# Kernel tuning notes

Measured on AMD Instinct MI355X. Metric: run time of the kernel, lower is better.

## Reference

```python
import jax, jax.numpy as jnp
import numpy as np

B, T, F_IN = 64, 396, 128
D_MODEL, N_HEAD, D_QKV, D_FF = 768, 8, 96, 3072
N_LAYERS, N_OUT, REL_D = 6, 256, 100


def setup_inputs():
    key = jax.random.key(0)
    cnt = [0]
    def rn(shape, std=1.0):
        cnt[0] += 1
        return jax.random.normal(jax.random.fold_in(key, cnt[0]), shape, jnp.float32) * std
    inp = {"x_raw": rn((B, T, F_IN))}
    def add_rb(p, cin, cout):
        inp[p + "_c1_w"] = rn((cout, cin, 3), (2.0 / (cin * 3)) ** 0.5)
        inp[p + "_c1_b"] = rn((cout,), 0.01)
        inp[p + "_bn1_s"] = 1.0 + rn((cout,), 0.1)
        inp[p + "_bn1_b"] = rn((cout,), 0.1)
        inp[p + "_c2_w"] = rn((cout, cout, 3), (2.0 / (cout * 3)) ** 0.5)
        inp[p + "_c2_b"] = rn((cout,), 0.01)
        inp[p + "_bn2_s"] = 1.0 + rn((cout,), 0.1)
        inp[p + "_bn2_b"] = rn((cout,), 0.1)
        inp[p + "_cr_w"] = rn((cout, cin, 1), (2.0 / cin) ** 0.5)
        inp[p + "_cr_b"] = rn((cout,), 0.01)
        inp[p + "_bnr_s"] = 1.0 + rn((cout,), 0.1)
        inp[p + "_bnr_b"] = rn((cout,), 0.1)
    add_rb("rb1", F_IN, D_MODEL)
    add_rb("rb2", D_MODEL, D_MODEL)
    inp["w_in_w"] = rn((D_MODEL, D_MODEL), D_MODEL ** -0.5)
    inp["w_in_b"] = rn((D_MODEL,), 0.01)
    inp["cls_token"] = jnp.zeros((1, 1, D_MODEL), jnp.float32)
    xav = (2.0 / (D_MODEL + D_QKV)) ** 0.5
    inp["wq"] = rn((N_LAYERS, N_HEAD, D_MODEL, D_QKV), xav)
    inp["wk"] = rn((N_LAYERS, N_HEAD, D_MODEL, D_QKV), xav)
    inp["wv"] = rn((N_LAYERS, N_HEAD, D_MODEL, D_QKV), xav)
    inp["wo"] = rn((N_LAYERS, N_HEAD, D_QKV, D_MODEL), xav)
    inp["rel_emb"] = rn((N_LAYERS, N_HEAD, 2 * REL_D + 1, D_QKV), D_QKV ** -0.5)
    inp["ln1_g"] = jnp.ones((N_LAYERS, D_MODEL), jnp.float32)
    inp["ln1_b"] = jnp.zeros((N_LAYERS, D_MODEL), jnp.float32)
    inp["ln2_g"] = jnp.ones((N_LAYERS, D_MODEL), jnp.float32)
    inp["ln2_b"] = jnp.zeros((N_LAYERS, D_MODEL), jnp.float32)
    inp["ff1_w"] = rn((N_LAYERS, D_FF, D_MODEL), (2.0 / D_MODEL) ** 0.5)
    inp["ff1_b"] = rn((N_LAYERS, D_FF), 0.01)
    inp["ff2_w"] = rn((N_LAYERS, D_MODEL, D_FF), (1.0 / D_FF) ** 0.5)
    inp["ff2_b"] = rn((N_LAYERS, D_MODEL), 0.01)
    inp["w_out_w"] = rn((N_OUT, D_MODEL), D_MODEL ** -0.5)
    inp["w_out_b"] = rn((N_OUT,), 0.01)
    return inp


def _conv1d(x, w, b, stride=1):
    # x: [B, Cin, T], w: [Cout, Cin, K]
    pad = (w.shape[-1] - 1) // 2
    y = jax.lax.conv_general_dilated(x, w, (stride,), [(pad, pad)],
                                     dimension_numbers=("NCH", "OIH", "NCH"))
    return y + b[None, :, None]


def _bn(x, s, b):
    # eval-mode BatchNorm1d folded into per-channel affine
    return x * s[None, :, None] + b[None, :, None]


def _resblock(x, c1w, c1b, s1, b1, c2w, c2b, s2, b2, crw, crb, sr, br, stride):
    h = jax.nn.relu(_bn(_conv1d(x, c1w, c1b, stride), s1, b1))
    h = _bn(_conv1d(h, c2w, c2b), s2, b2)
    r = _bn(_conv1d(x, crw, crb, stride), sr, br)
    return jax.nn.relu(h + r)


def _layer_norm(x, g, b, eps=1e-5):
    m = jnp.mean(x, -1, keepdims=True)
    v = jnp.mean((x - m) ** 2, -1, keepdims=True)
    return (x - m) * jax.lax.rsqrt(v + eps) * g + b


def _attention(x, wq, wk, wv, wo, rel):
    # x: [B, L, D]; relative-positional attention (fairseq LearnedRelativePositionalEmbedding, unmasked)
    L = x.shape[1]
    q = jnp.einsum("btf,hfa->bhta", x, wq) * (D_QKV ** -0.5)
    k = jnp.einsum("btf,hfa->bhta", x, wk)
    v = jnp.einsum("btf,hfa->bhta", x, wv)
    logits = jnp.einsum("bhqa,bhka->bhqk", q, k)
    # narrow embeddings to the 2L-1 relative positions used (L <= REL_D)
    start = REL_D - L
    rel_used = rel[:, start:start + 2 * L - 1, :]  # [h, 2L-1, a]
    pos_all = jnp.einsum("bhqa,hma->bhqm", q, rel_used)  # [B,h,L,2L-1]
    idx = jnp.arange(L)[None, :] - jnp.arange(L)[:, None] + (L - 1)  # [L,L], rel->abs skew
    logits = logits + jnp.take_along_axis(pos_all, idx[None, None], axis=3)
    probs = jax.nn.softmax(logits, axis=-1)
    o = jnp.einsum("bhqk,bhka->bhqa", probs, v)
    return jnp.einsum("bhta,haf->btf", o, wo)


def reference(x_raw, rb1_c1_w, rb1_c1_b, rb1_bn1_s, rb1_bn1_b, rb1_c2_w, rb1_c2_b, rb1_bn2_s, rb1_bn2_b, rb1_cr_w, rb1_cr_b, rb1_bnr_s, rb1_bnr_b, rb2_c1_w, rb2_c1_b, rb2_bn1_s, rb2_bn1_b, rb2_c2_w, rb2_c2_b, rb2_bn2_s, rb2_bn2_b, rb2_cr_w, rb2_cr_b, rb2_bnr_s, rb2_bnr_b, w_in_w, w_in_b, cls_token, wq, wk, wv, wo, rel_emb, ln1_g, ln1_b, ln2_g, ln2_b, ff1_w, ff1_b, ff2_w, ff2_b, w_out_w, w_out_b):
    x = jnp.transpose(x_raw, (0, 2, 1))  # [B, F_IN, T]
    x = _resblock(x, rb1_c1_w, rb1_c1_b, rb1_bn1_s, rb1_bn1_b, rb1_c2_w, rb1_c2_b, rb1_bn2_s, rb1_bn2_b, rb1_cr_w, rb1_cr_b, rb1_bnr_s, rb1_bnr_b, 2)
    x = _resblock(x, rb2_c1_w, rb2_c1_b, rb2_bn1_s, rb2_bn1_b, rb2_c2_w, rb2_c2_b, rb2_bn2_s, rb2_bn2_b, rb2_cr_w, rb2_cr_b, rb2_bnr_s, rb2_bnr_b, 2)
    x = jnp.transpose(x, (0, 2, 1))  # [B, T', D]
    x = x @ w_in_w.T + w_in_b
    cls = jnp.broadcast_to(cls_token, (x.shape[0], 1, D_MODEL))
    x = jnp.concatenate([cls, x], axis=1)  # [B, L, D], L = T'+1
    for l in range(N_LAYERS):
        a = _attention(x, wq[l], wk[l], wv[l], wo[l], rel_emb[l])
        x = _layer_norm(x + a, ln1_g[l], ln1_b[l])
        h = jax.nn.relu(x @ ff1_w[l].T + ff1_b[l]) @ ff2_w[l].T + ff2_b[l]
        x = _layer_norm(x + h, ln2_g[l], ln2_b[l])
    return x[:, 0, :] @ w_out_w.T + w_out_b
```

## Files before the change

kernel.cpp:

```cpp
#include <hip/hip_runtime.h>

typedef _Float16 h8 __attribute__((ext_vector_type(8)));
typedef float f4 __attribute__((ext_vector_type(4)));

namespace {

constexpr int DM   = 768;
constexpr int NHEAD= 8;
constexpr int DQ   = 96;
constexpr int DFF  = 3072;
constexpr int NL   = 6;
constexpr int B_   = 64;
constexpr int T0   = 396, T1 = 198, T2 = 99;
constexpr int FIN  = 128;
constexpr int L_   = 100;
constexpr int MSEQ = B_ * L_;
constexpr int M1   = B_ * T1;
constexpr int M2   = B_ * T2;
constexpr int NREL = 201;
constexpr int POSN = 256;
constexpr int RELK = 128;

enum { EPI_F32 = 0, EPI_RELU_H, EPI_H, EPI_CONV_BN_H, EPI_CONV_RELU_H, EPI_CONV_ADD_RELU_H };

__device__ __forceinline__ void g2l16(const _Float16* g, _Float16* l)
{
    __builtin_amdgcn_global_load_lds(
        (const __attribute__((address_space(1))) unsigned int*)g,
        (__attribute__((address_space(3))) unsigned int*)l,
        16, 0, 0);
}

template<int EPI, bool OPAD, int MI>
__device__ __forceinline__ void epilogue(
    f4 (&acc)[MI][4], int lane, int m0, int wm, int n0, int wn,
    int M, int N, int T_out, int bz,
    float* Cf, _Float16* Ch, const float* bias, const float* bns,
    const float* bnb, const _Float16* res, size_t c_z)
{
    const int frc = lane & 15;
    const int fq4 = (lane >> 4) * 4;
    float*    Cfo = Cf ? Cf + (size_t)bz * c_z : nullptr;
    _Float16* Cho = Ch ? Ch + (size_t)bz * c_z : nullptr;
    #pragma unroll
    for (int mi = 0; mi < MI; ++mi)
        #pragma unroll
        for (int ni = 0; ni < 4; ++ni)
            #pragma unroll
            for (int r = 0; r < 4; ++r) {
                int row = m0 + wm + mi * 16 + fq4 + r;
                int col = n0 + wn + ni * 16 + frc;
                if (row >= M) continue;
                float v = acc[mi][ni][r];
                size_t roff;
                if (OPAD) {
                    int ab = row / T_out, at = row - ab * T_out;
                    roff = ((size_t)ab * (T_out + 2) + at + 1) * N + col;
                } else {
                    roff = (size_t)row * N + col;
                }
                if (EPI == EPI_F32) {
                    if (bias) v += bias[col];
                    Cfo[roff] = v;
                } else if (EPI == EPI_RELU_H) {
                    if (bias) v += bias[col];
                    Cho[roff] = (_Float16)fmaxf(v, 0.0f);
                } else if (EPI == EPI_H) {
                    Cho[roff] = (_Float16)v;
                } else if (EPI == EPI_CONV_BN_H) {
                    v = bns[col] * (v + bias[col]) + bnb[col];
                    Cho[roff] = (_Float16)v;
                } else if (EPI == EPI_CONV_RELU_H) {
                    v = bns[col] * (v + bias[col]) + bnb[col];
                    Cho[roff] = (_Float16)fmaxf(v, 0.0f);
                } else {
                    v = bns[col] * (v + bias[col]) + bnb[col]
                      + (float)res[(size_t)row * N + col];
                    Cho[roff] = (_Float16)fmaxf(v, 0.0f);
                }
            }
}

template<int EPI, bool OPAD, int MI>
__global__ __launch_bounds__(256)
void gemm5_k(const _Float16* __restrict__ A, const _Float16* __restrict__ B,
             float* __restrict__ Cf, _Float16* __restrict__ Ch,
             const float* __restrict__ bias, const float* __restrict__ bns,
             const float* __restrict__ bnb, const _Float16* __restrict__ res,
             int M, int N, int K, int lda,
             int T_out, int Tp_in, int stride_t, int KS, int in_off,
             int gx, int gxy)
{
    constexpr int TM = MI * 32;
    __shared__ _Float16 As[TM * 64];
    __shared__ _Float16 Bs[128 * 64];

    const unsigned nwg = gridDim.x, orig = blockIdx.x;
    const unsigned q = nwg >> 3, rr_ = nwg & 7;
    const unsigned xcd = orig & 7, idx = orig >> 3;
    const unsigned wgid = (xcd < rr_) ? xcd * (q + 1) + idx
                                      : rr_ * (q + 1) + (xcd - rr_) * q + idx;
    const int by  = (int)(wgid / (unsigned)gx);
    const int bx  = (int)(wgid - (unsigned)by * (unsigned)gx);
    (void)gxy;

    const int tid  = threadIdx.x;
    const int lane = tid & 63;
    const int wid  = tid >> 6;
    const int m0   = by * TM;
    const int n0   = bx * 128;
    const int wm   = (wid >> 1) * (MI * 16);
    const int wn   = (wid & 1) * 64;

    f4 acc[MI][4];
    #pragma unroll
    for (int i = 0; i < MI; ++i)
        #pragma unroll
        for (int j = 0; j < 4; ++j)
            #pragma unroll
            for (int p = 0; p < 4; ++p) acc[i][j][p] = 0.0f;

    const int colh = (((lane & 7) ^ ((lane >> 3) & 7)) << 3);
    size_t aoff[MI];
    #pragma unroll
    for (int i = 0; i < MI; ++i) {
        int m = min(m0 + wid * (MI * 8) + i * 8 + (lane >> 3), M - 1);
        int ab = m / T_out, at = m - ab * T_out;
        aoff[i] = ((size_t)ab * Tp_in + at * stride_t + in_off) * lda + colh;
    }
    size_t boff[4];
    #pragma unroll
    for (int i = 0; i < 4; ++i)
        boff[i] = (size_t)(n0 + wid * 32 + i * 8 + (lane >> 3)) * K + colh;
    const size_t bdk = (size_t)N * K;

    const int fr  = lane & 15;
    const int grp = lane >> 4;

    for (int dk = 0; dk < KS; ++dk) {
        const size_t adk = (size_t)dk * lda;
        const size_t bdo = (size_t)dk * bdk;

        for (int k0 = 0; k0 < K; k0 += 64) {
            #pragma unroll
            for (int i = 0; i < MI; ++i)
                g2l16(A + aoff[i] + adk + k0, &As[(wid * (MI * 8) + i * 8) * 64]);
            #pragma unroll
            for (int i = 0; i < 4; ++i)
                g2l16(B + boff[i] + bdo + k0, &Bs[(wid * 32 + i * 8) * 64]);
            __syncthreads();

            #pragma unroll
            for (int kh = 0; kh < 2; ++kh) {
                const int co = (((kh * 4 + grp) ^ (fr & 7)) << 3);
                h8 af[MI], bf[4];
                #pragma unroll
                for (int mi = 0; mi < MI; ++mi)
                    af[mi] = *(const h8*)&As[(wm + mi * 16 + fr) * 64 + co];
                #pragma unroll
                for (int ni = 0; ni < 4; ++ni)
                    bf[ni] = *(const h8*)&Bs[(wn + ni * 16 + fr) * 64 + co];
                #pragma unroll
                for (int mi = 0; mi < MI; ++mi)
                    #pragma unroll
                    for (int ni = 0; ni < 4; ++ni)
                        acc[mi][ni] = __builtin_amdgcn_mfma_f32_16x16x32_f16(
                            af[mi], bf[ni], acc[mi][ni], 0, 0, 0);
            }
            __syncthreads();
        }
    }

    epilogue<EPI, OPAD, MI>(acc, lane, m0, wm, n0, wn, M, N, T_out, 0,
                            Cf, Ch, bias, bns, bnb, res, 0);
}

template<int EPI, int MI>
__global__ __launch_bounds__(256)
void gemm6_k(const _Float16* __restrict__ A, const _Float16* __restrict__ B,
             float* __restrict__ Cf, _Float16* __restrict__ Ch,
             const float* __restrict__ bias,
             int M, int N, int K, int lda,
             int gx, int gxy,
             size_t a_z, size_t b_z, size_t c_z)
{
    constexpr int TM = MI * 32;
    __shared__ _Float16 As[2][TM * 64];
    __shared__ _Float16 Bs[2][128 * 64];

    const unsigned nwg = gridDim.x, orig = blockIdx.x;
    const unsigned q = nwg >> 3, rr_ = nwg & 7;
    const unsigned xcd = orig & 7, idx = orig >> 3;
    const unsigned wgid = (xcd < rr_) ? xcd * (q + 1) + idx
                                      : rr_ * (q + 1) + (xcd - rr_) * q + idx;
    const int bz  = (int)(wgid / (unsigned)gxy);
    const int rem = (int)(wgid - (unsigned)bz * (unsigned)gxy);
    const int by  = rem / gx;
    const int bx  = rem - by * gx;

    A += (size_t)bz * a_z;
    B += (size_t)bz * b_z;

    const int tid  = threadIdx.x;
    const int lane = tid & 63;
    const int wid  = tid >> 6;
    const int m0   = by * TM;
    const int n0   = bx * 128;
    const int wm   = (wid >> 1) * (MI * 16);
    const int wn   = (wid & 1) * 64;

    f4 acc[MI][4];
    #pragma unroll
    for (int i = 0; i < MI; ++i)
        #pragma unroll
        for (int j = 0; j < 4; ++j)
            #pragma unroll
            for (int p = 0; p < 4; ++p) acc[i][j][p] = 0.0f;

    const int colh = (((lane & 7) ^ ((lane >> 3) & 7)) << 3);
    size_t aoff[MI];
    #pragma unroll
    for (int i = 0; i < MI; ++i) {
        int m = min(m0 + wid * (MI * 8) + i * 8 + (lane >> 3), M - 1);
        aoff[i] = (size_t)m * lda + colh;
    }
    size_t boff[4];
    #pragma unroll
    for (int i = 0; i < 4; ++i)
        boff[i] = (size_t)(n0 + wid * 32 + i * 8 + (lane >> 3)) * K + colh;

    const int fr  = lane & 15;
    const int grp = lane >> 4;
    const int NS  = K >> 6;

    auto stage = [&](int step, int buf) {
        const int k0 = step << 6;
        #pragma unroll
        for (int i = 0; i < MI; ++i)
            g2l16(A + aoff[i] + k0, &As[buf][(wid * (MI * 8) + i * 8) * 64]);
        #pragma unroll
        for (int i = 0; i < 4; ++i)
            g2l16(B + boff[i] + k0, &Bs[buf][(wid * 32 + i * 8) * 64]);
    };

    stage(0, 0);
    __syncthreads();

    for (int step = 0; step < NS; ++step) {
        const int cur = step & 1;
        const _Float16* As_ = As[cur];
        const _Float16* Bs_ = Bs[cur];

        const int co0 = ((grp ^ (fr & 7)) << 3);
        h8 af0[MI], bf0[4];
        #pragma unroll
        for (int mi = 0; mi < MI; ++mi)
            af0[mi] = *(const h8*)&As_[(wm + mi * 16 + fr) * 64 + co0];
        #pragma unroll
        for (int ni = 0; ni < 4; ++ni)
            bf0[ni] = *(const h8*)&Bs_[(wn + ni * 16 + fr) * 64 + co0];

        if (step + 1 < NS) stage(step + 1, cur ^ 1);

        #pragma unroll
        for (int mi = 0; mi < MI; ++mi)
            #pragma unroll
            for (int ni = 0; ni < 4; ++ni)
                acc[mi][ni] = __builtin_amdgcn_mfma_f32_16x16x32_f16(
                    af0[mi], bf0[ni], acc[mi][ni], 0, 0, 0);

        const int co1 = (((4 + grp) ^ (fr & 7)) << 3);
        h8 af1[MI], bf1[4];
        #pragma unroll
        for (int mi = 0; mi < MI; ++mi)
            af1[mi] = *(const h8*)&As_[(wm + mi * 16 + fr) * 64 + co1];
        #pragma unroll
        for (int ni = 0; ni < 4; ++ni)
            bf1[ni] = *(const h8*)&Bs_[(wn + ni * 16 + fr) * 64 + co1];
        #pragma unroll
        for (int mi = 0; mi < MI; ++mi)
            #pragma unroll
            for (int ni = 0; ni < 4; ++ni)
                acc[mi][ni] = __builtin_amdgcn_mfma_f32_16x16x32_f16(
                    af1[mi], bf1[ni], acc[mi][ni], 0, 0, 0);

        __syncthreads();
    }

    epilogue<EPI, false, MI>(acc, lane, m0, wm, n0, wn, M, N, 0, bz,
                             Cf, Ch, bias, nullptr, nullptr, nullptr, c_z);
}


__global__ void f2h_k(const float* __restrict__ in, _Float16* __restrict__ out,
                      long n, float scale)
{
    long i = (long)blockIdx.x * blockDim.x + threadIdx.x;
    if (i < n) out[i] = (_Float16)(in[i] * scale);
}

__global__ void f2h8_k(const float* __restrict__ in, _Float16* __restrict__ out,
                       long n8)
{
    long i = (long)blockIdx.x * blockDim.x + threadIdx.x;
    if (i >= n8) return;
    f4 a = ((const f4*)in)[2 * i];
    f4 b = ((const f4*)in)[2 * i + 1];
    h8 o;
    #pragma unroll
    for (int j = 0; j < 4; ++j) { o[j] = (_Float16)a[j]; o[4 + j] = (_Float16)b[j]; }
    ((h8*)out)[i] = o;
}

__global__ void f2h_pad_k(const float* __restrict__ in, _Float16* __restrict__ out)
{
    long i = (long)blockIdx.x * blockDim.x + threadIdx.x;
    if (i >= (long)B_ * 398 * FIN) return;
    int  c = (int)(i % FIN);
    long r = i / FIN;
    int  t = (int)(r % 398);
    int  b = (int)(r / 398);
    float v = (t == 0 || t == 397) ? 0.0f
            : in[((long)b * T0 + (t - 1)) * FIN + c];
    out[i] = (_Float16)v;
}

__global__ void zero_pad_k(_Float16* __restrict__ buf, int Tp, int C)
{
    long i = (long)blockIdx.x * blockDim.x + threadIdx.x;
    if (i >= (long)B_ * 2 * C) return;
    int  c = (int)(i % C);
    long r = i / C;
    int  hi = (int)(r % 2);
    int  b  = (int)(r / 2);
    buf[((size_t)b * Tp + (hi ? Tp - 1 : 0)) * C + c] = (_Float16)0.0f;
}

__global__ void pack_qkv_k(const float* __restrict__ wq, const float* __restrict__ wk,
                           const float* __restrict__ wv, _Float16* __restrict__ out)
{
    long i = (long)blockIdx.x * blockDim.x + threadIdx.x;
    if (i >= (long)NL * 2304 * DM) return;
    int  f = (int)(i % DM);
    long r = i / DM;
    int  n = (int)(r % 2304);
    int  l = (int)(r / 2304);
    int  s = n / DM, hn = n % DM, h = hn / DQ, a = hn % DQ;
    const float* src = (s == 0) ? wq : ((s == 1) ? wk : wv);
    out[i] = (_Float16)src[(((long)l * NHEAD + h) * DM + f) * DQ + a];
}

__global__ void pack_wo_k(const float* __restrict__ wo, _Float16* __restrict__ out)
{
    long i = (long)blockIdx.x * blockDim.x + threadIdx.x;
    if (i >= (long)NL * DM * DM) return;
    int  ha = (int)(i % DM);
    long r  = i / DM;
    int  f  = (int)(r % DM);
    int  l  = (int)(r / DM);
    int  h = ha / DQ, a = ha % DQ;
    out[i] = (_Float16)wo[(((long)l * NHEAD + h) * DQ + a) * DM + f];
}

__global__ void pack_conv_k(const float* __restrict__ w, _Float16* __restrict__ out,
                            int Cout, int Cin, int KS)
{
    long i = (long)blockIdx.x * blockDim.x + threadIdx.x;
    if (i >= (long)Cout * Cin * KS) return;
    int  ci = (int)(i % Cin);
    long r  = i / Cin;
    int  co = (int)(r % Cout);
    int  dk = (int)(r / Cout);
    out[i] = (_Float16)w[((long)co * Cin + ci) * KS + dk];
}

__global__ void pack_rel_k(const float* __restrict__ rel, _Float16* __restrict__ out)
{
    long i = (long)blockIdx.x * blockDim.x + threadIdx.x;
    if (i >= (long)NL * NHEAD * POSN * RELK) return;
    int  k = (int)(i & (RELK - 1));
    long r = i >> 7;
    int  n = (int)(r & (POSN - 1));
    long r2 = r >> 8;
    int  h = (int)(r2 & (NHEAD - 1));
    int  l = (int)(r2 >> 3);
    float v = 0.0f;
    if (n < NREL && k < DQ)
        v = rel[(((long)l * NHEAD + h) * NREL + n) * DQ + k] * 0.10206207261596575f;
    out[i] = (_Float16)v;
}

__global__ void concat_k(const float* __restrict__ xlin, const float* __restrict__ cls,
                         float* __restrict__ xf, _Float16* __restrict__ xh)
{
    long i = (long)blockIdx.x * blockDim.x + threadIdx.x;
    if (i >= (long)MSEQ * DM) return;
    int  c = (int)(i % DM);
    long m = i / DM;
    int  b = (int)(m / L_), t = (int)(m % L_);
    float v = (t == 0) ? cls[c] : xlin[((long)b * (L_ - 1) + (t - 1)) * DM + c];
    xf[i] = v;
    xh[i] = (_Float16)v;
}

__global__ __launch_bounds__(256)
void ln_k(const float* x, const float* __restrict__ d,
          const float* __restrict__ g, const float* __restrict__ bb,
          float* xo, _Float16* __restrict__ xh)
{
    long row = blockIdx.x;
    const float* xr = x + row * DM;
    const float* dr = d + row * DM;
    float v[3];
    float s = 0.0f;
    #pragma unroll
    for (int k = 0; k < 3; ++k) {
        int c = threadIdx.x + 256 * k;
        v[k] = xr[c] + dr[c];
        s += v[k];
    }
    __shared__ float red[8];
    #pragma unroll
    for (int o = 32; o; o >>= 1) s += __shfl_xor(s, o, 64);
    int w = threadIdx.x >> 6, lane = threadIdx.x & 63;
    if (lane == 0) red[w] = s;
    __syncthreads();
    s = red[0] + red[1] + red[2] + red[3];
    float mean = s * (1.0f / DM);
    float vs = 0.0f;
    #pragma unroll
    for (int k = 0; k < 3; ++k) { float t = v[k] - mean; vs += t * t; }
    #pragma unroll
    for (int o = 32; o; o >>= 1) vs += __shfl_xor(vs, o, 64);
    if (lane == 0) red[4 + w] = vs;
    __syncthreads();
    vs = red[4] + red[5] + red[6] + red[7];
    float rstd = rsqrtf(vs * (1.0f / DM) + 1e-5f);
    #pragma unroll
    for (int k = 0; k < 3; ++k) {
        int c = threadIdx.x + 256 * k;
        float y = (v[k] - mean) * rstd * g[c] + bb[c];
        xo[row * DM + c] = y;
        xh[row * DM + c] = (_Float16)y;
    }
}

constexpr int LP = 128;
constexpr int KP = 104;
constexpr int PP = 136;

__global__ __launch_bounds__(256)
void attn_k(const _Float16* __restrict__ qkv, const _Float16* __restrict__ pos,
            _Float16* __restrict__ o)
{
    __shared__ __align__(16) char smem[60928];
    _Float16* Ks = (_Float16*)smem;
    _Float16* Ps = (_Float16*)smem;
    _Float16* Vt = (_Float16*)(smem + 34816);

    const int h = blockIdx.x, b = blockIdx.y;
    const int tid = threadIdx.x, lane = tid & 63, w = tid >> 6;
    const _Float16* base = qkv + (size_t)b * L_ * 2304 + h * DQ;
    const float qscale = 0.10206207261596575f;

    {
        int row = tid >> 1;
        int c0  = (tid & 1) * 48;
        const bool real = row < L_;
        const _Float16* krow = base + 768 + (size_t)row * 2304;
        #pragma unroll
        for (int q = 0; q < 6; ++q) {
            int c = c0 + q * 8;
            h8 kv;
            #pragma unroll
            for (int e = 0; e < 8; ++e) kv[e] = (_Float16)0.0f;
            if (real) kv = *(const h8*)(krow + c);
            *(h8*)&Ks[row * KP + c] = kv;
        }
        for (int idx = tid; idx < DQ * LP; idx += 256) {
            int a = idx % DQ, j = idx / DQ;
            _Float16 v = (_Float16)0.0f;
            if (j < L_) v = base[1536 + (size_t)j * 2304 + a];
            Vt[a * PP + j] = v;
        }
    }
    __syncthreads();

    const int fr = lane & 15;
    const int fk = (lane >> 4) * 8;
    const int rbase = w * 32 + ((lane >> 4) << 2);

    f4 acc[2][8];
    #pragma unroll
    for (int mi = 0; mi < 2; ++mi)
        #pragma unroll
        for (int ni = 0; ni < 8; ++ni)
            #pragma unroll
            for (int q = 0; q < 4; ++q) acc[mi][ni][q] = 0.0f;

    #pragma unroll
    for (int k0 = 0; k0 < DQ; k0 += 32) {
        h8 a0 = *(const h8*)(base + (size_t)(w * 32 + fr) * 2304 + k0 + fk);
        h8 a1 = *(const h8*)(base + (size_t)(w * 32 + 16 + fr) * 2304 + k0 + fk);
        #pragma unroll
        for (int ni = 0; ni < 8; ++ni) {
            h8 bv = *(const h8*)&Ks[(ni * 16 + fr) * KP + k0 + fk];
            acc[0][ni] = __builtin_amdgcn_mfma_f32_16x16x32_f16(a0, bv, acc[0][ni], 0, 0, 0);
            acc[1][ni] = __builtin_amdgcn_mfma_f32_16x16x32_f16(a1, bv, acc[1][ni], 0, 0, 0);
        }
    }

    const _Float16* posb = pos + ((size_t)h * MSEQ + (size_t)b * L_) * POSN;
    #pragma unroll
    for (int mi = 0; mi < 2; ++mi)
        #pragma unroll
        for (int r = 0; r < 4; ++r) {
            int i = rbase + mi * 16 + r;
            float s[8];
            #pragma unroll
            for (int ni = 0; ni < 8; ++ni) {
                int j = ni * 16 + fr;
                float v = -3.0e38f;
                if (i < L_ && j < L_)
                    v = acc[mi][ni][r] * qscale
                      + (float)posb[(size_t)i * POSN + (j - i + (L_ - 1))];
                s[ni] = v;
            }
            float m = s[0];
            #pragma unroll
            for (int ni = 1; ni < 8; ++ni) m = fmaxf(m, s[ni]);
            #pragma unroll
            for (int msk = 1; msk < 16; msk <<= 1) m = fmaxf(m, __shfl_xor(m, msk, 64));
            float sum = 0.0f;
            #pragma unroll
            for (int ni = 0; ni < 8; ++ni) { s[ni] = __expf(s[ni] - m); sum += s[ni]; }
            #pragma unroll
            for (int msk = 1; msk < 16; msk <<= 1) sum += __shfl_xor(sum, msk, 64);
            float inv = 1.0f / sum;
            #pragma unroll
            for (int ni = 0; ni < 8; ++ni) acc[mi][ni][r] = s[ni] * inv;
        }

    __syncthreads();

    #pragma unroll
    for (int mi = 0; mi < 2; ++mi)
        #pragma unroll
        for (int r = 0; r < 4; ++r) {
            int i = rbase + mi * 16 + r;
            #pragma unroll
            for (int ni = 0; ni < 8; ++ni)
                Ps[i * PP + ni * 16 + fr] = (_Float16)acc[mi][ni][r];
        }
    __syncthreads();

    f4 acc2[2][6];
    #pragma unroll
    for (int mi = 0; mi < 2; ++mi)
        #pragma unroll
        for (int ni = 0; ni < 6; ++ni)
            #pragma unroll
            for (int q = 0; q < 4; ++q) acc2[mi][ni][q] = 0.0f;

    #pragma unroll
    for (int k0 = 0; k0 < LP; k0 += 32) {
        h8 a0 = *(const h8*)&Ps[(w * 32 + fr) * PP + k0 + fk];
        h8 a1 = *(const h8*)&Ps[(w * 32 + 16 + fr) * PP + k0 + fk];
        #pragma unroll
        for (int ni = 0; ni < 6; ++ni) {
            h8 bv = *(const h8*)&Vt[(ni * 16 + fr) * PP + k0 + fk];
            acc2[0][ni] = __builtin_amdgcn_mfma_f32_16x16x32_f16(a0, bv, acc2[0][ni], 0, 0, 0);
            acc2[1][ni] = __builtin_amdgcn_mfma_f32_16x16x32_f16(a1, bv, acc2[1][ni], 0, 0, 0);
        }
    }

    _Float16* ob = o + (size_t)b * L_ * DM + h * DQ;
    #pragma unroll
    for (int mi = 0; mi < 2; ++mi)
        #pragma unroll
        for (int r = 0; r < 4; ++r) {
            int i = rbase + mi * 16 + r;
            if (i < L_) {
                #pragma unroll
                for (int ni = 0; ni < 6; ++ni)
                    ob[(size_t)i * DM + ni * 16 + fr] = (_Float16)acc2[mi][ni][r];
            }
        }
}

__global__ __launch_bounds__(256)
void out_k(const float* __restrict__ xseq, const float* __restrict__ w,
           const float* __restrict__ bias, float* __restrict__ out)
{
    __shared__ float xs[DM];
    int b = blockIdx.x;
    for (int c = threadIdx.x; c < DM; c += 256) xs[c] = xseq[(size_t)b * L_ * DM + c];
    __syncthreads();
    int n = threadIdx.x;
    const f4* wr = (const f4*)(w + (size_t)n * DM);
    float acc = 0.0f;
    #pragma unroll 4
    for (int k4 = 0; k4 < DM / 4; ++k4) {
        f4 wv = wr[k4];
        f4 xv = *(const f4*)&xs[k4 * 4];
        acc += wv[0]*xv[0] + wv[1]*xv[1] + wv[2]*xv[2] + wv[3]*xv[3];
    }
    out[(size_t)b * 256 + n] = acc + bias[n];
}

}

extern "C" void kernel_launch(void* const* d_in, const int* in_sizes, int n_in,
                              void* d_out, int out_size, void* d_ws, size_t ws_size,
                              hipStream_t stream)
{
    (void)in_sizes; (void)n_in; (void)out_size; (void)ws_size;

    const float* x_raw   = (const float*)d_in[0];
    const float* rb1_c1w = (const float*)d_in[1];
    const float* rb1_c1b = (const float*)d_in[2];
    const float* rb1_s1  = (const float*)d_in[3];
    const float* rb1_b1  = (const float*)d_in[4];
    const float* rb1_c2w = (const float*)d_in[5];
    const float* rb1_c2b = (const float*)d_in[6];
    const float* rb1_s2  = (const float*)d_in[7];
    const float* rb1_b2  = (const float*)d_in[8];
    const float* rb1_crw = (const float*)d_in[9];
    const float* rb1_crb = (const float*)d_in[10];
    const float* rb1_sr  = (const float*)d_in[11];
    const float* rb1_br  = (const float*)d_in[12];
    const float* rb2_c1w = (const float*)d_in[13];
    const float* rb2_c1b = (const float*)d_in[14];
    const float* rb2_s1  = (const float*)d_in[15];
    const float* rb2_b1  = (const float*)d_in[16];
    const float* rb2_c2w = (const float*)d_in[17];
    const float* rb2_c2b = (const float*)d_in[18];
    const float* rb2_s2  = (const float*)d_in[19];
    const float* rb2_b2  = (const float*)d_in[20];
    const float* rb2_crw = (const float*)d_in[21];
    const float* rb2_crb = (const float*)d_in[22];
    const float* rb2_sr  = (const float*)d_in[23];
    const float* rb2_br  = (const float*)d_in[24];
    const float* w_in_w  = (const float*)d_in[25];
    const float* w_in_b  = (const float*)d_in[26];
    const float* cls     = (const float*)d_in[27];
    const float* wq      = (const float*)d_in[28];
    const float* wk      = (const float*)d_in[29];
    const float* wv      = (const float*)d_in[30];
    const float* wo      = (const float*)d_in[31];
    const float* rel     = (const float*)d_in[32];
    const float* ln1g    = (const float*)d_in[33];
    const float* ln1b    = (const float*)d_in[34];
    const float* ln2g    = (const float*)d_in[35];
    const float* ln2b    = (const float*)d_in[36];
    const float* ff1w    = (const float*)d_in[37];
    const float* ff1b    = (const float*)d_in[38];
    const float* ff2w    = (const float*)d_in[39];
    const float* ff2b    = (const float*)d_in[40];
    const float* w_out_w = (const float*)d_in[41];
    const float* w_out_b = (const float*)d_in[42];

    char* base = (char*)d_ws;
    size_t off = 0;
    auto carve = [&](size_t bytes) -> char* {
        char* p = base + off;
        off = (off + bytes + 255) & ~(size_t)255;
        return p;
    };
    _Float16* w_in_h = (_Float16*)carve((size_t)589824 * 2);
    _Float16* qkvw   = (_Float16*)carve((size_t)10616832 * 2);
    _Float16* wow    = (_Float16*)carve((size_t)3538944 * 2);
    _Float16* ff1h   = (_Float16*)carve((size_t)14155776 * 2);
    _Float16* ff2h   = (_Float16*)carve((size_t)14155776 * 2);
    _Float16* relh   = (_Float16*)carve((size_t)NL * NHEAD * POSN * RELK * 2);
    _Float16* cw11   = (_Float16*)carve((size_t)294912 * 2);
    _Float16* cw12   = (_Float16*)carve((size_t)1769472 * 2);
    _Float16* cw1r   = (_Float16*)carve((size_t)98304 * 2);
    _Float16* cw21   = (_Float16*)carve((size_t)1769472 * 2);
    _Float16* cw22   = (_Float16*)carve((size_t)1769472 * 2);
    _Float16* cw2r   = (_Float16*)carve((size_t)589824 * 2);
    _Float16* xrawp  = (_Float16*)carve((size_t)B_ * 398 * FIN * 2);
    float*    xseq_f = (float*)carve((size_t)4915200 * 4);
    _Float16* xseq_h = (_Float16*)carve((size_t)4915200 * 2);
    _Float16* qkvb   = (_Float16*)carve((size_t)14745600 * 2);
    _Float16* ohb    = (_Float16*)carve((size_t)4915200 * 2);
    float*    af     = (float*)carve((size_t)4915200 * 4);
    char*     hhreg  = carve((size_t)19660800 * 2);
    float*    yf     = (float*)carve((size_t)4915200 * 4);
    _Float16* h1_rb1 = qkvb;
    _Float16* r_rb1h = (_Float16*)hhreg;
    _Float16* out1   = (_Float16*)af;
    _Float16* h1_rb2 = (_Float16*)xseq_f;
    _Float16* r_rb2h = (_Float16*)yf;
    _Float16* out2   = ohb;
    float*    xlin   = (float*)hhreg;
    _Float16* posh   = (_Float16*)hhreg;
    _Float16* ffh    = (_Float16*)hhreg;

    dim3 blk(256, 1, 1);
    auto grd = [](long n) { return dim3((unsigned)((n + 255) / 256), 1, 1); };
    #define NWG(M, N, TM, GZ) dim3((unsigned)(((N) / 128) * (((M) + (TM) - 1) / (TM)) * (GZ)), 1, 1)
    #define GXY(M, N, TM) ((N) / 128), (((N) / 128) * (((M) + (TM) - 1) / (TM)))

    f2h_pad_k<<<grd((long)B_ * 398 * FIN), blk, 0, stream>>>(x_raw, xrawp);
    zero_pad_k<<<grd((long)B_ * 2 * DM), blk, 0, stream>>>(h1_rb1, 200, DM);
    zero_pad_k<<<grd((long)B_ * 2 * DM), blk, 0, stream>>>(out1, 200, DM);
    zero_pad_k<<<grd((long)B_ * 2 * DM), blk, 0, stream>>>(h1_rb2, 101, DM);
    f2h8_k<<<grd(589824 / 8), blk, 0, stream>>>(w_in_w, w_in_h, 589824 / 8);
    f2h8_k<<<grd(14155776 / 8), blk, 0, stream>>>(ff1w, ff1h, 14155776 / 8);
    f2h8_k<<<grd(14155776 / 8), blk, 0, stream>>>(ff2w, ff2h, 14155776 / 8);
    pack_rel_k<<<grd((long)NL * NHEAD * POSN * RELK), blk, 0, stream>>>(rel, relh);
    pack_qkv_k<<<grd((long)NL * 2304 * DM), blk, 0, stream>>>(wq, wk, wv, qkvw);
    pack_wo_k<<<grd((long)NL * DM * DM), blk, 0, stream>>>(wo, wow);
    pack_conv_k<<<grd(294912), blk, 0, stream>>>(rb1_c1w, cw11, DM, FIN, 3);
    pack_conv_k<<<grd(1769472), blk, 0, stream>>>(rb1_c2w, cw12, DM, DM, 3);
    pack_conv_k<<<grd(98304), blk, 0, stream>>>(rb1_crw, cw1r, DM, FIN, 1);
    pack_conv_k<<<grd(1769472), blk, 0, stream>>>(rb2_c1w, cw21, DM, DM, 3);
    pack_conv_k<<<grd(1769472), blk, 0, stream>>>(rb2_c2w, cw22, DM, DM, 3);
    pack_conv_k<<<grd(589824), blk, 0, stream>>>(rb2_crw, cw2r, DM, DM, 1);

    gemm5_k<EPI_CONV_BN_H, false, 4><<<NWG(M1, DM, 128, 1), blk, 0, stream>>>(
        xrawp, cw1r, nullptr, r_rb1h, rb1_crb, rb1_sr, rb1_br, nullptr,
        M1, DM, FIN, FIN, T1, 398, 2, 1, 1, GXY(M1, DM, 128));
    gemm5_k<EPI_CONV_RELU_H, true, 4><<<NWG(M1, DM, 128, 1), blk, 0, stream>>>(
        xrawp, cw11, nullptr, h1_rb1, rb1_c1b, rb1_s1, rb1_b1, nullptr,
        M1, DM, FIN, FIN, T1, 398, 2, 3, 0, GXY(M1, DM, 128));
    gemm5_k<EPI_CONV_ADD_RELU_H, true, 4><<<NWG(M1, DM, 128, 1), blk, 0, stream>>>(
        h1_rb1, cw12, nullptr, out1, rb1_c2b, rb1_s2, rb1_b2, r_rb1h,
        M1, DM, DM, DM, T1, 200, 1, 3, 0, GXY(M1, DM, 128));

    gemm5_k<EPI_CONV_BN_H, false, 2><<<NWG(M2, DM, 64, 1), blk, 0, stream>>>(
        out1, cw2r, nullptr, r_rb2h, rb2_crb, rb2_sr, rb2_br, nullptr,
        M2, DM, DM, DM, T2, 200, 2, 1, 1, GXY(M2, DM, 64));
    gemm5_k<EPI_CONV_RELU_H, true, 2><<<NWG(M2, DM, 64, 1), blk, 0, stream>>>(
        out1, cw21, nullptr, h1_rb2, rb2_c1b, rb2_s1, rb2_b1, nullptr,
        M2, DM, DM, DM, T2, 200, 2, 3, 0, GXY(M2, DM, 64));
    gemm5_k<EPI_CONV_ADD_RELU_H, false, 2><<<NWG(M2, DM, 64, 1), blk, 0, stream>>>(
        h1_rb2, cw22, nullptr, out2, rb2_c2b, rb2_s2, rb2_b2, r_rb2h,
        M2, DM, DM, DM, T2, 101, 1, 3, 0, GXY(M2, DM, 64));

    gemm6_k<EPI_F32, 2><<<NWG(M2, DM, 64, 1), blk, 0, stream>>>(
        out2, w_in_h, xlin, nullptr, w_in_b,
        M2, DM, DM, DM, GXY(M2, DM, 64), 0, 0, 0);
    concat_k<<<grd((long)MSEQ * DM), blk, 0, stream>>>(xlin, cls, xseq_f, xseq_h);

    for (int l = 0; l < NL; ++l) {
        gemm6_k<EPI_H, 4><<<NWG(MSEQ, 2304, 128, 1), blk, 0, stream>>>(
            xseq_h, qkvw + (size_t)l * 2304 * DM, nullptr, qkvb, nullptr,
            MSEQ, 2304, DM, DM, GXY(MSEQ, 2304, 128), 0, 0, 0);
        gemm6_k<EPI_H, 4><<<NWG(MSEQ, POSN, 128, NHEAD), blk, 0, stream>>>(
            qkvb, relh + (size_t)l * NHEAD * POSN * RELK, nullptr, posh, nullptr,
            MSEQ, POSN, RELK, 2304, GXY(MSEQ, POSN, 128),
            (size_t)DQ, (size_t)POSN * RELK, (size_t)MSEQ * POSN);
        attn_k<<<dim3(NHEAD, B_, 1), blk, 0, stream>>>(qkvb, posh, ohb);
        gemm6_k<EPI_F32, 2><<<NWG(MSEQ, DM, 64, 1), blk, 0, stream>>>(
            ohb, wow + (size_t)l * DM * DM, af, nullptr, nullptr,
            MSEQ, DM, DM, DM, GXY(MSEQ, DM, 64), 0, 0, 0);
        ln_k<<<dim3(MSEQ), blk, 0, stream>>>(xseq_f, af, ln1g + l * DM, ln1b + l * DM,
                                             xseq_f, xseq_h);
        gemm6_k<EPI_RELU_H, 4><<<NWG(MSEQ, DFF, 128, 1), blk, 0, stream>>>(
            xseq_h, ff1h + (size_t)l * DFF * DM, nullptr, ffh, ff1b + l * DFF,
            MSEQ, DFF, DM, DM, GXY(MSEQ, DFF, 128), 0, 0, 0);
        gemm6_k<EPI_F32, 2><<<NWG(MSEQ, DM, 64, 1), blk, 0, stream>>>(
            ffh, ff2h + (size_t)l * DM * DFF, yf, nullptr, ff2b + l * DM,
            MSEQ, DM, DFF, DFF, GXY(MSEQ, DM, 64), 0, 0, 0);
        ln_k<<<dim3(MSEQ), blk, 0, stream>>>(xseq_f, yf, ln2g + l * DM, ln2b + l * DM,
                                             xseq_f, xseq_h);
    }

    out_k<<<dim3(B_), blk, 0, stream>>>(xseq_f, w_out_w, w_out_b, (float*)d_out);
    #undef NWG
    #undef GXY
}
```

Before: 1.943 ms.

## Add 4-stage async-copy pipelined GEMM kernel for transformer layer matmuls

Adds a new GEMM kernel that stages 32-wide K slices into a 4-slot shared-memory ring with direct global-to-LDS copies, keeping three stages in flight via explicit vmcnt waits, and uses XOR-swizzled LDS columns. It also remaps workgroup IDs across XCDs for locality. The QKV, output-projection and both FFN GEMMs in each layer switch to it, aiming to hide global load latency behind MFMA work. The hand-written waitcnt counts depend on how many loads are issued per stage, so the barrier logic is fragile. The unused f2h_k kernel is removed.

```diff
diff --git a/kernel.cpp b/kernel.cpp
--- a/kernel.cpp
+++ b/kernel.cpp
@@ -291,13 +291,114 @@
                              Cf, Ch, bias, nullptr, nullptr, nullptr, c_z);
 }
 
-
-__global__ void f2h_k(const float* __restrict__ in, _Float16* __restrict__ out,
-                      long n, float scale)
-{
-    long i = (long)blockIdx.x * blockDim.x + threadIdx.x;
-    if (i < n) out[i] = (_Float16)(in[i] * scale);
-}
+template<int EPI, int MI>
+__global__ __launch_bounds__(256)
+void gemm7_k(const _Float16* __restrict__ A, const _Float16* __restrict__ B,
+             float* __restrict__ Cf, _Float16* __restrict__ Ch,
+             const float* __restrict__ bias,
+             int M, int N, int K, int lda,
+             int gx, int gxy)
+{
+    constexpr int TM   = MI * 32;
+    constexpr int AI   = TM / 64;
+    constexpr int LPS  = AI + 2;
+    constexpr int SLOT = (TM + 128) * 32;
+    __shared__ _Float16 S[4 * SLOT];
+
+    const unsigned nwg = gridDim.x, orig = blockIdx.x;
+    const unsigned q = nwg >> 3, rr_ = nwg & 7;
+    const unsigned xcd = orig & 7, idx = orig >> 3;
+    const unsigned wgid = (xcd < rr_) ? xcd * (q + 1) + idx
+                                      : rr_ * (q + 1) + (xcd - rr_) * q + idx;
+    const int by  = (int)(wgid / (unsigned)gx);
+    const int bx  = (int)(wgid - (unsigned)by * (unsigned)gx);
+    (void)gxy;
+
+    const int tid  = threadIdx.x;
+    const int lane = tid & 63;
+    const int wid  = tid >> 6;
+    const int m0   = by * TM;
+    const int n0   = bx * 128;
+    const int wm   = (wid >> 1) * (MI * 16);
+    const int wn   = (wid & 1) * 64;
+
+    f4 acc[MI][4];
+    #pragma unroll
+    for (int i = 0; i < MI; ++i)
+        #pragma unroll
+        for (int j = 0; j < 4; ++j)
+            #pragma unroll
+            for (int p = 0; p < 4; ++p) acc[i][j][p] = 0.0f;
+
+    const int srow  = wid * 16 + (lane >> 2);
+    const int colh  = (((lane & 3) ^ ((lane >> 2) & 3)) << 3);
+    size_t aoff[AI];
+    #pragma unroll
+    for (int i = 0; i < AI; ++i) {
+        int m = min(m0 + i * 64 + srow, M - 1);
+        aoff[i] = (size_t)m * lda + colh;
+    }
+    size_t boff[2];
+    #pragma unroll
+    for (int i = 0; i < 2; ++i)
+        boff[i] = (size_t)(n0 + i * 64 + srow) * K + colh;
+
+    const int fr  = lane & 15;
+    const int grp = lane >> 4;
+    const int NS  = K >> 5;
+
+    auto stage = [&](int t) {
+        const int k0   = t << 5;
+        _Float16* sb   = &S[(size_t)(t & 3) * SLOT];
+        #pragma unroll
+        for (int i = 0; i < AI; ++i)
+            g2l16(A + aoff[i] + k0, sb + (i * 64 + wid * 16) * 32);
+        #pragma unroll
+        for (int i = 0; i < 2; ++i)
+            g2l16(B + boff[i] + k0, sb + TM * 32 + (i * 64 + wid * 16) * 32);
+    };
+
+    for (int i = 0; i < 3 && i < NS; ++i) stage(i);
+
+    for (int t = 0; t < NS; ++t) {
+        if (t + 3 < NS) {
+            stage(t + 3);
+            if constexpr (LPS == 4)
+                asm volatile("s_waitcnt vmcnt(12)" ::: "memory");
+            else
+                asm volatile("s_waitcnt vmcnt(9)" ::: "memory");
+        } else {
+            asm volatile("s_waitcnt vmcnt(0)" ::: "memory");
+        }
+        __builtin_amdgcn_s_barrier();
+        __builtin_amdgcn_sched_barrier(0);
+
+        const _Float16* Ss = &S[(size_t)(t & 3) * SLOT];
+        const int co = ((grp ^ (fr & 3)) << 3);
+        h8 af[MI], bf[4];
+        #pragma unroll
+        for (int mi = 0; mi < MI; ++mi)
+            af[mi] = *(const h8*)&Ss[(wm + mi * 16 + fr) * 32 + co];
+        #pragma unroll
+        for (int ni = 0; ni < 4; ++ni)
+            bf[ni] = *(const h8*)&Ss[TM * 32 + (wn + ni * 16 + fr) * 32 + co];
+        #pragma unroll
+        for (int mi = 0; mi < MI; ++mi)
+            #pragma unroll
+            for (int ni = 0; ni < 4; ++ni)
+                acc[mi][ni] = __builtin_amdgcn_mfma_f32_16x16x32_f16(
+                    af[mi], bf[ni], acc[mi][ni], 0, 0, 0);
+
+        asm volatile("s_waitcnt lgkmcnt(0)" ::: "memory");
+        __builtin_amdgcn_sched_barrier(0);
+        __builtin_amdgcn_s_barrier();
+        __builtin_amdgcn_sched_barrier(0);
+    }
+
+    epilogue<EPI, false, MI>(acc, lane, m0, wm, n0, wn, M, N, 0, 0,
+                             Cf, Ch, bias, nullptr, nullptr, nullptr, 0);
+}
+
 
 __global__ void f2h8_k(const float* __restrict__ in, _Float16* __restrict__ out,
                        long n8)
@@ -745,25 +846,25 @@
     concat_k<<<grd((long)MSEQ * DM), blk, 0, stream>>>(xlin, cls, xseq_f, xseq_h);
 
     for (int l = 0; l < NL; ++l) {
-        gemm6_k<EPI_H, 4><<<NWG(MSEQ, 2304, 128, 1), blk, 0, stream>>>(
+        gemm7_k<EPI_H, 4><<<NWG(MSEQ, 2304, 128, 1), blk, 0, stream>>>(
             xseq_h, qkvw + (size_t)l * 2304 * DM, nullptr, qkvb, nullptr,
-            MSEQ, 2304, DM, DM, GXY(MSEQ, 2304, 128), 0, 0, 0);
+            MSEQ, 2304, DM, DM, GXY(MSEQ, 2304, 128));
         gemm6_k<EPI_H, 4><<<NWG(MSEQ, POSN, 128, NHEAD), blk, 0, stream>>>(
             qkvb, relh + (size_t)l * NHEAD * POSN * RELK, nullptr, posh, nullptr,
             MSEQ, POSN, RELK, 2304, GXY(MSEQ, POSN, 128),
             (size_t)DQ, (size_t)POSN * RELK, (size_t)MSEQ * POSN);
         attn_k<<<dim3(NHEAD, B_, 1), blk, 0, stream>>>(qkvb, posh, ohb);
-        gemm6_k<EPI_F32, 2><<<NWG(MSEQ, DM, 64, 1), blk, 0, stream>>>(
+        gemm7_k<EPI_F32, 2><<<NWG(MSEQ, DM, 64, 1), blk, 0, stream>>>(
             ohb, wow + (size_t)l * DM * DM, af, nullptr, nullptr,
-            MSEQ, DM, DM, DM, GXY(MSEQ, DM, 64), 0, 0, 0);
+            MSEQ, DM, DM, DM, GXY(MSEQ, DM, 64));
         ln_k<<<dim3(MSEQ), blk, 0, stream>>>(xseq_f, af, ln1g + l * DM, ln1b + l * DM,
                                              xseq_f, xseq_h);
-        gemm6_k<EPI_RELU_H, 4><<<NWG(MSEQ, DFF, 128, 1), blk, 0, stream>>>(
+        gemm7_k<EPI_RELU_H, 4><<<NWG(MSEQ, DFF, 128, 1), blk, 0, stream>>>(
             xseq_h, ff1h + (size_t)l * DFF * DM, nullptr, ffh, ff1b + l * DFF,
-            MSEQ, DFF, DM, DM, GXY(MSEQ, DFF, 128), 0, 0, 0);
-        gemm6_k<EPI_F32, 2><<<NWG(MSEQ, DM, 64, 1), blk, 0, stream>>>(
+            MSEQ, DFF, DM, DM, GXY(MSEQ, DFF, 128));
+        gemm7_k<EPI_F32, 2><<<NWG(MSEQ, DM, 64, 1), blk, 0, stream>>>(
             ffh, ff2h + (size_t)l * DM * DFF, yf, nullptr, ff2b + l * DM,
-            MSEQ, DM, DFF, DFF, GXY(MSEQ, DM, 64), 0, 0, 0);
+            MSEQ, DM, DFF, DFF, GXY(MSEQ, DM, 64));
         ln_k<<<dim3(MSEQ), blk, 0, stream>>>(xseq_f, yf, ln2g + l * DM, ln2b + l * DM,
                                              xseq_f, xseq_h);
     }
```

Result: slower. 2.048 ms (+5.4%).

## Add 128x256 single-buffered GEMM for QKV/FF1 and fuse residual add into GEMM epilogue

Applied to the files above, without the earlier changes.

Adds a new GEMM kernel with a 128x256 output tile, where each wave computes 64x128, and uses it for the QKV projection and the FF1 projection. The larger tile is meant to raise arithmetic intensity and MFMA work per LDS load. Its LDS use is single-buffered and it holds 128 accumulator registers per lane, which may lower occupancy and lose overlap. Separately, the Wo and FF2 GEMMs now add the fp32 residual in their epilogue, so the layer-norm kernel reads one input array instead of two.

```diff
diff --git a/kernel.cpp b/kernel.cpp
--- a/kernel.cpp
+++ b/kernel.cpp
@@ -21,7 +21,8 @@
 constexpr int POSN = 256;
 constexpr int RELK = 128;
 
-enum { EPI_F32 = 0, EPI_RELU_H, EPI_H, EPI_CONV_BN_H, EPI_CONV_RELU_H, EPI_CONV_ADD_RELU_H };
+enum { EPI_F32 = 0, EPI_RELU_H, EPI_H, EPI_CONV_BN_H, EPI_CONV_RELU_H,
+       EPI_CONV_ADD_RELU_H, EPI_ADD_F32 };
 
 __device__ __forceinline__ void g2l16(const _Float16* g, _Float16* l)
 {
@@ -31,12 +32,12 @@
         16, 0, 0);
 }
 
-template<int EPI, bool OPAD, int MI>
+template<int EPI, bool OPAD, int MI, int NI>
 __device__ __forceinline__ void epilogue(
-    f4 (&acc)[MI][4], int lane, int m0, int wm, int n0, int wn,
+    f4 (&acc)[MI][NI], int lane, int m0, int wm, int n0, int wn,
     int M, int N, int T_out, int bz,
     float* Cf, _Float16* Ch, const float* bias, const float* bns,
-    const float* bnb, const _Float16* res, size_t c_z)
+    const float* bnb, const _Float16* res, const float* resf, size_t c_z)
 {
     const int frc = lane & 15;
     const int fq4 = (lane >> 4) * 4;
@@ -45,7 +46,7 @@
     #pragma unroll
     for (int mi = 0; mi < MI; ++mi)
         #pragma unroll
-        for (int ni = 0; ni < 4; ++ni)
+        for (int ni = 0; ni < NI; ++ni)
             #pragma unroll
             for (int r = 0; r < 4; ++r) {
                 int row = m0 + wm + mi * 16 + fq4 + r;
@@ -61,6 +62,10 @@
                 }
                 if (EPI == EPI_F32) {
                     if (bias) v += bias[col];
+                    Cfo[roff] = v;
+                } else if (EPI == EPI_ADD_F32) {
+                    if (bias) v += bias[col];
+                    v += resf[(size_t)row * N + col];
                     Cfo[roff] = v;
                 } else if (EPI == EPI_RELU_H) {
                     if (bias) v += bias[col];
@@ -171,15 +176,15 @@
         }
     }
 
-    epilogue<EPI, OPAD, MI>(acc, lane, m0, wm, n0, wn, M, N, T_out, 0,
-                            Cf, Ch, bias, bns, bnb, res, 0);
+    epilogue<EPI, OPAD, MI, 4>(acc, lane, m0, wm, n0, wn, M, N, T_out, 0,
+                               Cf, Ch, bias, bns, bnb, res, nullptr, 0);
 }
 
 template<int EPI, int MI>
 __global__ __launch_bounds__(256)
 void gemm6_k(const _Float16* __restrict__ A, const _Float16* __restrict__ B,
              float* __restrict__ Cf, _Float16* __restrict__ Ch,
-             const float* __restrict__ bias,
+             const float* __restrict__ bias, const float* __restrict__ resf,
              int M, int N, int K, int lda,
              int gx, int gxy,
              size_t a_z, size_t b_z, size_t c_z)
@@ -287,17 +292,92 @@
         __syncthreads();
     }
 
-    epilogue<EPI, false, MI>(acc, lane, m0, wm, n0, wn, M, N, 0, bz,
-                             Cf, Ch, bias, nullptr, nullptr, nullptr, c_z);
-}
-
-
-__global__ void f2h_k(const float* __restrict__ in, _Float16* __restrict__ out,
-                      long n, float scale)
-{
-    long i = (long)blockIdx.x * blockDim.x + threadIdx.x;
-    if (i < n) out[i] = (_Float16)(in[i] * scale);
-}
+    epilogue<EPI, false, MI, 4>(acc, lane, m0, wm, n0, wn, M, N, 0, bz,
+                                Cf, Ch, bias, nullptr, nullptr, nullptr, resf, c_z);
+}
+
+template<int EPI>
+__global__ __launch_bounds__(256)
+void gemm8_k(const _Float16* __restrict__ A, const _Float16* __restrict__ B,
+             float* __restrict__ Cf, _Float16* __restrict__ Ch,
+             const float* __restrict__ bias,
+             int M, int N, int K, int lda, int gx)
+{
+    __shared__ _Float16 As[128 * 64];
+    __shared__ _Float16 Bs[256 * 64];
+
+    const unsigned nwg = gridDim.x, orig = blockIdx.x;
+    const unsigned q = nwg >> 3, rr_ = nwg & 7;
+    const unsigned xcd = orig & 7, idx = orig >> 3;
+    const unsigned wgid = (xcd < rr_) ? xcd * (q + 1) + idx
+                                      : rr_ * (q + 1) + (xcd - rr_) * q + idx;
+    const int by  = (int)(wgid / (unsigned)gx);
+    const int bx  = (int)(wgid - (unsigned)by * (unsigned)gx);
+
+    const int tid  = threadIdx.x;
+    const int lane = tid & 63;
+    const int wid  = tid >> 6;
+    const int m0   = by * 128;
+    const int n0   = bx * 256;
+    const int wm   = (wid >> 1) * 64;
+    const int wn   = (wid & 1) * 128;
+
+    f4 acc[4][8];
+    #pragma unroll
+    for (int i = 0; i < 4; ++i)
+        #pragma unroll
+        for (int j = 0; j < 8; ++j)
+            #pragma unroll
+            for (int p = 0; p < 4; ++p) acc[i][j][p] = 0.0f;
+
+    const int colh = (((lane & 7) ^ ((lane >> 3) & 7)) << 3);
+    size_t aoff[4];
+    #pragma unroll
+    for (int i = 0; i < 4; ++i) {
+        int m = min(m0 + wid * 32 + i * 8 + (lane >> 3), M - 1);
+        aoff[i] = (size_t)m * lda + colh;
+    }
+    size_t boff[8];
+    #pragma unroll
+    for (int i = 0; i < 8; ++i)
+        boff[i] = (size_t)(n0 + wid * 64 + i * 8 + (lane >> 3)) * K + colh;
+
+    const int fr  = lane & 15;
+    const int grp = lane >> 4;
+
+    for (int k0 = 0; k0 < K; k0 += 64) {
+        #pragma unroll
+        for (int i = 0; i < 4; ++i)
+            g2l16(A + aoff[i] + k0, &As[(wid * 32 + i * 8) * 64]);
+        #pragma unroll
+        for (int i = 0; i < 8; ++i)
+            g2l16(B + boff[i] + k0, &Bs[(wid * 64 + i * 8) * 64]);
+        __syncthreads();
+
+        #pragma unroll
+        for (int kh = 0; kh < 2; ++kh) {
+            const int co = (((kh * 4 + grp) ^ (fr & 7)) << 3);
+            h8 af[4], bf[8];
+            #pragma unroll
+            for (int mi = 0; mi < 4; ++mi)
+                af[mi] = *(const h8*)&As[(wm + mi * 16 + fr) * 64 + co];
+            #pragma unroll
+            for (int ni = 0; ni < 8; ++ni)
+                bf[ni] = *(const h8*)&Bs[(wn + ni * 16 + fr) * 64 + co];
+            #pragma unroll
+            for (int mi = 0; mi < 4; ++mi)
+                #pragma unroll
+                for (int ni = 0; ni < 8; ++ni)
+                    acc[mi][ni] = __builtin_amdgcn_mfma_f32_16x16x32_f16(
+                        af[mi], bf[ni], acc[mi][ni], 0, 0, 0);
+        }
+        __syncthreads();
+    }
+
+    epilogue<EPI, false, 4, 8>(acc, lane, m0, wm, n0, wn, M, N, 0, 0,
+                               Cf, Ch, bias, nullptr, nullptr, nullptr, nullptr, 0);
+}
+
 
 __global__ void f2h8_k(const float* __restrict__ in, _Float16* __restrict__ out,
                        long n8)
@@ -404,19 +484,18 @@
 }
 
 __global__ __launch_bounds__(256)
-void ln_k(const float* x, const float* __restrict__ d,
+void ln_k(const float* __restrict__ sIn,
           const float* __restrict__ g, const float* __restrict__ bb,
-          float* xo, _Float16* __restrict__ xh)
+          float* __restrict__ xo, _Float16* __restrict__ xh)
 {
     long row = blockIdx.x;
-    const float* xr = x + row * DM;
-    const float* dr = d + row * DM;
+    const float* sr = sIn + row * DM;
     float v[3];
     float s = 0.0f;
     #pragma unroll
     for (int k = 0; k < 3; ++k) {
         int c = threadIdx.x + 256 * k;
-        v[k] = xr[c] + dr[c];
+        v[k] = sr[c];
         s += v[k];
     }
     __shared__ float red[8];
@@ -701,6 +780,7 @@
     auto grd = [](long n) { return dim3((unsigned)((n + 255) / 256), 1, 1); };
     #define NWG(M, N, TM, GZ) dim3((unsigned)(((N) / 128) * (((M) + (TM) - 1) / (TM)) * (GZ)), 1, 1)
     #define GXY(M, N, TM) ((N) / 128), (((N) / 128) * (((M) + (TM) - 1) / (TM)))
+    #define NWG8(M, N) dim3((unsigned)(((N) / 256) * ((M) / 128)), 1, 1)
 
     f2h_pad_k<<<grd((long)B_ * 398 * FIN), blk, 0, stream>>>(x_raw, xrawp);
     zero_pad_k<<<grd((long)B_ * 2 * DM), blk, 0, stream>>>(h1_rb1, 200, DM);
@@ -740,35 +820,36 @@
         M2, DM, DM, DM, T2, 101, 1, 3, 0, GXY(M2, DM, 64));
 
     gemm6_k<EPI_F32, 2><<<NWG(M2, DM, 64, 1), blk, 0, stream>>>(
-        out2, w_in_h, xlin, nullptr, w_in_b,
+        out2, w_in_h, xlin, nullptr, w_in_b, nullptr,
         M2, DM, DM, DM, GXY(M2, DM, 64), 0, 0, 0);
     concat_k<<<grd((long)MSEQ * DM), blk, 0, stream>>>(xlin, cls, xseq_f, xseq_h);
 
     for (int l = 0; l < NL; ++l) {
-        gemm6_k<EPI_H, 4><<<NWG(MSEQ, 2304, 128, 1), blk, 0, stream>>>(
+        gemm8_k<EPI_H><<<NWG8(MSEQ, 2304), blk, 0, stream>>>(
             xseq_h, qkvw + (size_t)l * 2304 * DM, nullptr, qkvb, nullptr,
-            MSEQ, 2304, DM, DM, GXY(MSEQ, 2304, 128), 0, 0, 0);
+            MSEQ, 2304, DM, DM, 2304 / 256);
         gemm6_k<EPI_H, 4><<<NWG(MSEQ, POSN, 128, NHEAD), blk, 0, stream>>>(
-            qkvb, relh + (size_t)l * NHEAD * POSN * RELK, nullptr, posh, nullptr,
+            qkvb, relh + (size_t)l * NHEAD * POSN * RELK, nullptr, posh, nullptr, nullptr,
             MSEQ, POSN, RELK, 2304, GXY(MSEQ, POSN, 128),
             (size_t)DQ, (size_t)POSN * RELK, (size_t)MSEQ * POSN);
         attn_k<<<dim3(NHEAD, B_, 1), blk, 0, stream>>>(qkvb, posh, ohb);
-        gemm6_k<EPI_F32, 2><<<NWG(MSEQ, DM, 64, 1), blk, 0, stream>>>(
-            ohb, wow + (size_t)l * DM * DM, af, nullptr, nullptr,
+        gemm6_k<EPI_ADD_F32, 2><<<NWG(MSEQ, DM, 64, 1), blk, 0, stream>>>(
+            ohb, wow + (size_t)l * DM * DM, af, nullptr, nullptr, xseq_f,
             MSEQ, DM, DM, DM, GXY(MSEQ, DM, 64), 0, 0, 0);
-        ln_k<<<dim3(MSEQ), blk, 0, stream>>>(xseq_f, af, ln1g + l * DM, ln1b + l * DM,
+        ln_k<<<dim3(MSEQ), blk, 0, stream>>>(af, ln1g + l * DM, ln1b + l * DM,
                                              xseq_f, xseq_h);
-        gemm6_k<EPI_RELU_H, 4><<<NWG(MSEQ, DFF, 128, 1), blk, 0, stream>>>(
+        gemm8_k<EPI_RELU_H><<<NWG8(MSEQ, DFF), blk, 0, stream>>>(
             xseq_h, ff1h + (size_t)l * DFF * DM, nullptr, ffh, ff1b + l * DFF,
-            MSEQ, DFF, DM, DM, GXY(MSEQ, DFF, 128), 0, 0, 0);
-        gemm6_k<EPI_F32, 2><<<NWG(MSEQ, DM, 64, 1), blk, 0, stream>>>(
-            ffh, ff2h + (size_t)l * DM * DFF, yf, nullptr, ff2b + l * DM,
+            MSEQ, DFF, DM, DM, DFF / 256);
+        gemm6_k<EPI_ADD_F32, 2><<<NWG(MSEQ, DM, 64, 1), blk, 0, stream>>>(
+            ffh, ff2h + (size_t)l * DM * DFF, yf, nullptr, ff2b + l * DM, xseq_f,
             MSEQ, DM, DFF, DFF, GXY(MSEQ, DM, 64), 0, 0, 0);
-        ln_k<<<dim3(MSEQ), blk, 0, stream>>>(xseq_f, yf, ln2g + l * DM, ln2b + l * DM,
+        ln_k<<<dim3(MSEQ), blk, 0, stream>>>(yf, ln2g + l * DM, ln2b + l * DM,
                                              xseq_f, xseq_h);
     }
 
     out_k<<<dim3(B_), blk, 0, stream>>>(xseq_f, w_out_w, w_out_b, (float*)d_out);
     #undef NWG
     #undef GXY
-}
+    #undef NWG8
+}
```

After: 2.483 ms. +27.8%, slower.
